# Kernel optimization log

Hardware: AMD Instinct MI355X
Metric: run time of the kernel (lower is better)

The kernel has to match this reference:

```python
import jax, jax.numpy as jnp
import numpy as np

B, T, E, H = 2, 2048, 1024, 16
DV = E // H
EPS = 1e-5

def _layernorm(x, g, b):
    m = jnp.mean(x, axis=-1, keepdims=True)
    v = jnp.mean((x - m) ** 2, axis=-1, keepdims=True)
    return (x - m) * jax.lax.rsqrt(v + EPS) * g + b

def setup_inputs() -> dict:
    key = jax.random.key(0)
    ks = jax.random.split(key, 10)
    s = lambda fan_in: 1.0 / np.sqrt(fan_in)
    return {
        "x": jax.random.normal(ks[0], (B, T, E), jnp.float32),
        "wq": jax.random.normal(ks[1], (H, E, DV), jnp.float32) * s(E),
        "wk": jax.random.normal(ks[2], (H, E, DV), jnp.float32) * s(E),
        "wv": jax.random.normal(ks[3], (H, E, DV), jnp.float32) * s(E),
        "w_proj": jax.random.normal(ks[4], (E, E), jnp.float32) * s(E),
        "b_proj": jnp.zeros((E,), jnp.float32),
        "w1": jax.random.normal(ks[5], (E, 4 * E), jnp.float32) * s(E),
        "b1": jnp.zeros((4 * E,), jnp.float32),
        "w2": jax.random.normal(ks[6], (4 * E, E), jnp.float32) * s(4 * E),
        "b2": jnp.zeros((E,), jnp.float32),
        "g1": jnp.ones((E,), jnp.float32),
        "be1": jnp.zeros((E,), jnp.float32),
        "g2": jnp.ones((E,), jnp.float32),
        "be2": jnp.zeros((E,), jnp.float32),
    }

def reference(x, wq, wk, wv, w_proj, b_proj, w1, b1, w2, b2, g1, be1, g2, be2):
    Bc, Tc, C = x.shape
    # --- masked multi-head self-attention on pre-LN input ---
    h = _layernorm(x, g1, be1)
    q = jnp.einsum('bte,hed->bhtd', h, wq)
    k = jnp.einsum('bte,hed->bhtd', h, wk)
    v = jnp.einsum('bte,hed->bhtd', h, wv)
    # NOTE: original scales by C**-0.5 where C = full embed dim (not head dim)
    scores = jnp.einsum('bhtd,bhsd->bhts', q, k) * (C ** -0.5)
    causal = jnp.tril(jnp.ones((Tc, Tc), bool))
    scores = jnp.where(causal, scores, jnp.float32(-jnp.inf))
    probs = jax.nn.softmax(scores, axis=-1)  # dropout is identity in eval
    attn = jnp.einsum('bhts,bhsd->bhtd', probs, v)
    attn = attn.transpose(0, 2, 1, 3).reshape(Bc, Tc, C)
    x = x + (attn @ w_proj + b_proj)
    # --- feed-forward ---
    h2 = _layernorm(x, g2, be2)
    ff = jax.nn.relu(h2 @ w1 + b1) @ w2 + b2
    return x + ff
```

## Files before the change

### kernel.cpp

```cpp
#include <hip/hip_runtime.h>
#include <hip/hip_bf16.h>

typedef __bf16 bf16x8 __attribute__((ext_vector_type(8)));
typedef __bf16 bf16x4 __attribute__((ext_vector_type(4)));
typedef float f32x4 __attribute__((ext_vector_type(4)));

#define T_SEQ 2048
#define EMB 1024
#define NH 16
#define DV 64

__device__ __forceinline__ void gload16(const __bf16* g, __bf16* l) {
    __builtin_amdgcn_global_load_lds(
        (const __attribute__((address_space(1))) unsigned int*)g,
        (__attribute__((address_space(3))) unsigned int*)l, 16, 0, 0);
}

__global__ void transpose_cvt(const float* __restrict__ src, __bf16* __restrict__ dst,
                              int R, int C, long src_bstride, long dst_bstride, float scale) {
    __shared__ float tile[32][33];
    const int b = blockIdx.z;
    const float* s = src + (long)b * src_bstride;
    __bf16* d = dst + (long)b * dst_bstride;
    const int c0 = blockIdx.x * 32, r0 = blockIdx.y * 32;
    #pragma unroll
    for (int i = threadIdx.y; i < 32; i += 8)
        tile[i][threadIdx.x] = s[(long)(r0 + i) * C + c0 + threadIdx.x];
    __syncthreads();
    #pragma unroll
    for (int i = threadIdx.y; i < 32; i += 8)
        d[(long)(c0 + i) * R + r0 + threadIdx.x] = (__bf16)(tile[threadIdx.x][i] * scale);
}

__global__ void vt_transpose(const __bf16* __restrict__ qkv, __bf16* __restrict__ Vt) {
    __shared__ __bf16 tile[64][72];
    const int bh = blockIdx.y, b = bh >> 4, h = bh & 15;
    const int t0 = blockIdx.x * 64;
    const __bf16* src = qkv + (long)b * T_SEQ * 3072 + 2048 + h * 64;
    const int tt = threadIdx.x >> 3, seg = threadIdx.x & 7;
    #pragma unroll
    for (int half = 0; half < 2; half++) {
        const int t = half * 32 + tt;
        bf16x8 v = *reinterpret_cast<const bf16x8*>(src + (long)(t0 + t) * 3072 + seg * 8);
        *reinterpret_cast<bf16x8*>(&tile[t][seg * 8]) = v;
    }
    __syncthreads();
    __bf16* dst = Vt + (long)bh * 64 * T_SEQ + t0;
    #pragma unroll
    for (int half = 0; half < 2; half++) {
        const int d = half * 32 + tt;
        bf16x8 v;
        #pragma unroll
        for (int i = 0; i < 8; i++) v[i] = tile[seg * 8 + i][d];
        *reinterpret_cast<bf16x8*>(dst + (long)d * T_SEQ + seg * 8) = v;
    }
}

__global__ void ln_kernel(const float* __restrict__ x, const float* __restrict__ g,
                          const float* __restrict__ be, __bf16* __restrict__ out) {
    const int row = blockIdx.x;
    const float4 xv = reinterpret_cast<const float4*>(x + (long)row * EMB)[threadIdx.x];
    float s = xv.x + xv.y + xv.z + xv.w;
    float sq = xv.x * xv.x + xv.y * xv.y + xv.z * xv.z + xv.w * xv.w;
    #pragma unroll
    for (int off = 32; off; off >>= 1) { s += __shfl_down(s, off); sq += __shfl_down(sq, off); }
    __shared__ float red[8];
    const int w = threadIdx.x >> 6, lane = threadIdx.x & 63;
    if (lane == 0) { red[w] = s; red[4 + w] = sq; }
    __syncthreads();
    if (threadIdx.x == 0) {
        float st = red[0] + red[1] + red[2] + red[3];
        float sqt = red[4] + red[5] + red[6] + red[7];
        float mean = st * (1.0f / EMB);
        float var = sqt * (1.0f / EMB) - mean * mean;
        red[0] = mean; red[1] = rsqrtf(var + 1e-5f);
    }
    __syncthreads();
    const float mean = red[0], rstd = red[1];
    const float4 gv = reinterpret_cast<const float4*>(g)[threadIdx.x];
    const float4 bv = reinterpret_cast<const float4*>(be)[threadIdx.x];
    bf16x4 o;
    o[0] = (__bf16)((xv.x - mean) * rstd * gv.x + bv.x);
    o[1] = (__bf16)((xv.y - mean) * rstd * gv.y + bv.y);
    o[2] = (__bf16)((xv.z - mean) * rstd * gv.z + bv.z);
    o[3] = (__bf16)((xv.w - mean) * rstd * gv.w + bv.w);
    *reinterpret_cast<bf16x4*>(out + (long)row * EMB + threadIdx.x * 4) = o;
}

template <int BN, int OUT_BF16, int RELU, int HAS_BIAS, int HAS_RES>
__global__ __launch_bounds__(256)
void gemm_nt(const __bf16* __restrict__ A, const __bf16* __restrict__ BT,
             const float* __restrict__ bias, const float* __restrict__ res,
             void* __restrict__ outp, int M, int N, int K) {
    constexpr int NFN = BN / 32;
    __shared__ __align__(16) __bf16 As[128 * 64];
    __shared__ __align__(16) __bf16 Bs[BN * 64];
    const int t = threadIdx.x;
    const int w = t >> 6, lane = t & 63;
    const int wm = (w >> 1) * 64, wn = (w & 1) * (BN / 2);
    const int m0 = blockIdx.y * 128, n0 = blockIdx.x * BN;
    const int rA = lane & 15, kA = (lane >> 4) * 8;
    const int srow = t >> 3;
    const int scol = (t & 7) * 8;

    const __bf16* Ab = A + (long)(m0 + srow) * K + scol;
    const __bf16* Bb = BT + (long)(n0 + srow) * K + scol;
    __bf16* Asw = As + srow * 64 + scol;
    __bf16* Bsw = Bs + srow * 64 + scol;

    f32x4 acc[4][NFN] = {};
    for (int k0 = 0; k0 < K; k0 += 64) {
        #pragma unroll
        for (int i = 0; i < 4; i++)
            gload16(Ab + (long)(32 * i) * K + k0, Asw + 32 * i * 64);
        #pragma unroll
        for (int i = 0; i < BN / 32; i++)
            gload16(Bb + (long)(32 * i) * K + k0, Bsw + 32 * i * 64);
        __syncthreads();
        #pragma unroll
        for (int kk = 0; kk < 2; kk++) {
            bf16x8 af[4], bfr[NFN];
            #pragma unroll
            for (int m = 0; m < 4; m++)
                af[m] = *reinterpret_cast<const bf16x8*>(As + (wm + m * 16 + rA) * 64 + kk * 32 + kA);
            #pragma unroll
            for (int n = 0; n < NFN; n++)
                bfr[n] = *reinterpret_cast<const bf16x8*>(Bs + (wn + n * 16 + rA) * 64 + kk * 32 + kA);
            #pragma unroll
            for (int m = 0; m < 4; m++)
                #pragma unroll
                for (int n = 0; n < NFN; n++)
                    acc[m][n] = __builtin_amdgcn_mfma_f32_16x16x32_bf16(af[m], bfr[n], acc[m][n], 0, 0, 0);
        }
        __syncthreads();
    }
    const int rl = (lane >> 4) * 4, cl = lane & 15;
    #pragma unroll
    for (int m = 0; m < 4; m++) {
        #pragma unroll
        for (int n = 0; n < NFN; n++) {
            const int gc = n0 + wn + n * 16 + cl;
            float bval = 0.0f;
            if (HAS_BIAS) bval = bias[gc];
            #pragma unroll
            for (int r = 0; r < 4; r++) {
                const int gr = m0 + wm + m * 16 + rl + r;
                float v = acc[m][n][r] + bval;
                if (HAS_RES) v += res[(long)gr * N + gc];
                if (RELU) v = fmaxf(v, 0.0f);
                if (OUT_BF16) ((__bf16*)outp)[(long)gr * N + gc] = (__bf16)v;
                else          ((float*)outp)[(long)gr * N + gc] = v;
            }
        }
    }
}

template <int MASKED>
__device__ __forceinline__ void attn_compute(
    const char* __restrict__ Kl, const char* __restrict__ Vl,
    __bf16 (*__restrict__ PsW)[72],
    const bf16x8 (&qf)[2][2], const bf16x8& ones,
    f32x4 (&o)[2][4], f32x4 (&l5)[2], float (&mr)[2][4],
    int kv0, int rA, int g, int rl, int qw)
{
    const int swz = (rA & 7) << 4;
    bf16x8 kf[4][2];
    #pragma unroll
    for (int c = 0; c < 4; c++)
        #pragma unroll
        for (int kc = 0; kc < 2; kc++)
            kf[c][kc] = *reinterpret_cast<const bf16x8*>(
                Kl + (c * 16 + rA) * 128 + ((kc * 64 + g * 16) ^ swz));
    f32x4 sa[2][4];
    #pragma unroll
    for (int rt = 0; rt < 2; rt++)
        #pragma unroll
        for (int c = 0; c < 4; c++) {
            f32x4 acc = {};
            acc = __builtin_amdgcn_mfma_f32_16x16x32_bf16(qf[rt][0], kf[c][0], acc, 0, 0, 0);
            acc = __builtin_amdgcn_mfma_f32_16x16x32_bf16(qf[rt][1], kf[c][1], acc, 0, 0, 0);
            sa[rt][c] = acc;
        }
    #pragma unroll
    for (int rt = 0; rt < 2; rt++) {
        #pragma unroll
        for (int r = 0; r < 4; r++) {
            float s0 = sa[rt][0][r], s1 = sa[rt][1][r], s2 = sa[rt][2][r], s3 = sa[rt][3][r];
            if (MASKED) {
                const int gr = qw + rt * 16 + rl + r;
                if (kv0 + rA > gr)      s0 = -__builtin_inff();
                if (kv0 + 16 + rA > gr) s1 = -__builtin_inff();
                if (kv0 + 32 + rA > gr) s2 = -__builtin_inff();
                if (kv0 + 48 + rA > gr) s3 = -__builtin_inff();
            }
            float tm = fmaxf(fmaxf(s0, s1), fmaxf(s2, s3));
            #pragma unroll
            for (int msk = 1; msk < 16; msk <<= 1) tm = fmaxf(tm, __shfl_xor(tm, msk));
            const float mo = mr[rt][r];
            const float mn = fmaxf(mo, tm);
            mr[rt][r] = mn;
            const float sc = __expf(mo - mn);
            const float p0 = __expf(s0 - mn);
            const float p1 = __expf(s1 - mn);
            const float p2 = __expf(s2 - mn);
            const float p3 = __expf(s3 - mn);
            #pragma unroll
            for (int n = 0; n < 4; n++) o[rt][n][r] *= sc;
            l5[rt][r] *= sc;
            const int prow = rt * 16 + rl + r;
            PsW[prow][rA]      = (__bf16)p0;
            PsW[prow][16 + rA] = (__bf16)p1;
            PsW[prow][32 + rA] = (__bf16)p2;
            PsW[prow][48 + rA] = (__bf16)p3;
        }
    }
    asm volatile("s_waitcnt lgkmcnt(0)" ::: "memory");

    bf16x8 ap[2][2];
    #pragma unroll
    for (int rt = 0; rt < 2; rt++)
        #pragma unroll
        for (int ks = 0; ks < 2; ks++)
            ap[rt][ks] = *reinterpret_cast<const bf16x8*>(&PsW[rt * 16 + rA][ks * 32 + g * 8]);
    #pragma unroll
    for (int ks = 0; ks < 2; ks++) {
        #pragma unroll
        for (int rt = 0; rt < 2; rt++)
            l5[rt] = __builtin_amdgcn_mfma_f32_16x16x32_bf16(ap[rt][ks], ones, l5[rt], 0, 0, 0);
        #pragma unroll
        for (int n = 0; n < 4; n++) {
            bf16x8 bv = *reinterpret_cast<const bf16x8*>(
                Vl + (n * 16 + rA) * 128 + ((ks * 64 + g * 16) ^ swz));
            #pragma unroll
            for (int rt = 0; rt < 2; rt++)
                o[rt][n] = __builtin_amdgcn_mfma_f32_16x16x32_bf16(ap[rt][ks], bv, o[rt][n], 0, 0, 0);
        }
    }
}

__global__ __launch_bounds__(256)
void attn_kernel(const __bf16* __restrict__ qkv, const __bf16* __restrict__ Vt,
                 __bf16* __restrict__ attn) {
    __shared__ __bf16 Ks[2][64 * 64];
    __shared__ __bf16 Vs[2][64 * 64];
    __shared__ __bf16 Ps[4][32][72];

    const int bh = blockIdx.y, b = bh >> 4, h = bh & 15;
    const int qtile = (int)gridDim.x - 1 - (int)blockIdx.x;
    const int q0 = qtile * 128;
    const int w = threadIdx.x >> 6, lane = threadIdx.x & 63;
    const int qw = q0 + w * 32;
    const int rA = lane & 15, g = lane >> 4, rl = g * 4;
    const int srow8 = lane >> 3;
    const int scol = (lane & 7) * 16;
    const int wcol = scol ^ (srow8 << 4);

    const char* qb = (const char*)(qkv + (long)b * T_SEQ * 3072 + h * 64);
    const char* kb = qb + 2048;
    const char* vtb = (const char*)(Vt + (long)bh * 64 * T_SEQ);

    bf16x8 qf[2][2];
    #pragma unroll
    for (int rt = 0; rt < 2; rt++)
        #pragma unroll
        for (int kc = 0; kc < 2; kc++)
            qf[rt][kc] = *reinterpret_cast<const bf16x8*>(
                qb + (long)(qw + rt * 16 + rA) * 6144 + kc * 64 + g * 16);

    bf16x8 ones;
    #pragma unroll
    for (int i = 0; i < 8; i++) ones[i] = (__bf16)1.0f;

    f32x4 o[2][4] = {};
    f32x4 l5[2] = {};
    float mr[2][4];
    #pragma unroll
    for (int rt = 0; rt < 2; rt++)
        #pragma unroll
        for (int r = 0; r < 4; r++) mr[rt][r] = -__builtin_inff();

    const int nsteps = q0 / 64 + 2;
    const int t_avail = qw + 32;
    const int isK = (w < 2);
    const int r0 = (w & 1) * 32 + srow8;

    bf16x8 stg[4];
    auto issue = [&](int kv0) {
        if (isK) {
            #pragma unroll
            for (int i = 0; i < 4; i++)
                stg[i] = *reinterpret_cast<const bf16x8*>(kb + (long)(kv0 + r0 + i * 8) * 6144 + scol);
        } else {
            #pragma unroll
            for (int i = 0; i < 4; i++)
                stg[i] = *reinterpret_cast<const bf16x8*>(vtb + (long)(r0 + i * 8) * 4096 + kv0 * 2 + scol);
        }
    };
    auto lwrite = [&](int buf) {
        char* base = isK ? (char*)Ks[buf] : (char*)Vs[buf];
        #pragma unroll
        for (int i = 0; i < 4; i++)
            *reinterpret_cast<bf16x8*>(base + (r0 + i * 8) * 128 + wcol) = stg[i];
    };

    issue(0);
    lwrite(0);
    __syncthreads();

    for (int t = 0; t < nsteps; ++t) {
        const int kv0 = t * 64, cur = t & 1;
        const bool has_next = (t + 1 < nsteps);
        if (has_next) issue(kv0 + 64);
        if (kv0 < t_avail) {
            if (kv0 + 64 <= qw)
                attn_compute<0>((const char*)Ks[cur], (const char*)Vs[cur], Ps[w],
                                qf, ones, o, l5, mr, kv0, rA, g, rl, qw);
            else
                attn_compute<1>((const char*)Ks[cur], (const char*)Vs[cur], Ps[w],
                                qf, ones, o, l5, mr, kv0, rA, g, rl, qw);
        }
        if (has_next) lwrite(cur ^ 1);
        __syncthreads();
    }

    #pragma unroll
    for (int rt = 0; rt < 2; rt++)
        #pragma unroll
        for (int n = 0; n < 4; n++)
            #pragma unroll
            for (int r = 0; r < 4; r++) {
                const int gr = qw + rt * 16 + rl + r;
                attn[(long)(b * T_SEQ + gr) * EMB + h * 64 + n * 16 + rA] =
                    (__bf16)(o[rt][n][r] / l5[rt][r]);
            }
}

extern "C" void kernel_launch(void* const* d_in, const int* in_sizes, int n_in,
                              void* d_out, int out_size, void* d_ws, size_t ws_size,
                              hipStream_t stream) {
    const float* x      = (const float*)d_in[0];
    const float* wq     = (const float*)d_in[1];
    const float* wk     = (const float*)d_in[2];
    const float* wv     = (const float*)d_in[3];
    const float* w_proj = (const float*)d_in[4];
    const float* b_proj = (const float*)d_in[5];
    const float* w1     = (const float*)d_in[6];
    const float* b1     = (const float*)d_in[7];
    const float* w2     = (const float*)d_in[8];
    const float* b2     = (const float*)d_in[9];
    const float* g1     = (const float*)d_in[10];
    const float* be1    = (const float*)d_in[11];
    const float* g2     = (const float*)d_in[12];
    const float* be2    = (const float*)d_in[13];
    float* out = (float*)d_out;

    char* ws = (char*)d_ws;
    __bf16* WqkvT = (__bf16*)ws;  ws += 3072L * 1024 * 2;
    __bf16* WprojT = (__bf16*)ws; ws += 1024L * 1024 * 2;
    __bf16* W1T = (__bf16*)ws;    ws += 4096L * 1024 * 2;
    __bf16* W2T = (__bf16*)ws;    ws += 1024L * 4096 * 2;
    __bf16* h1  = (__bf16*)ws;    ws += 4096L * 1024 * 2;
    __bf16* qkvb = (__bf16*)ws;
    __bf16* attnb = (__bf16*)(ws + 4096L * 3072 * 2);
    __bf16* ffb = (__bf16*)ws;    ws += 4096L * 3072 * 2 + 4096L * 1024 * 2;
    float* x2 = (float*)ws;
    __bf16* Vt = (__bf16*)ws;

    const dim3 tb(32, 8);
    transpose_cvt<<<dim3(2, 32, 16), tb, 0, stream>>>(wq, WqkvT,                1024, 64, 65536L, 65536L, 0.03125f);
    transpose_cvt<<<dim3(2, 32, 16), tb, 0, stream>>>(wk, WqkvT + 1024L * 1024, 1024, 64, 65536L, 65536L, 1.0f);
    transpose_cvt<<<dim3(2, 32, 16), tb, 0, stream>>>(wv, WqkvT + 2048L * 1024, 1024, 64, 65536L, 65536L, 1.0f);
    transpose_cvt<<<dim3(32, 32, 1),  tb, 0, stream>>>(w_proj, WprojT, 1024, 1024, 0, 0, 1.0f);
    transpose_cvt<<<dim3(128, 32, 1), tb, 0, stream>>>(w1, W1T, 1024, 4096, 0, 0, 1.0f);
    transpose_cvt<<<dim3(32, 128, 1), tb, 0, stream>>>(w2, W2T, 4096, 1024, 0, 0, 1.0f);

    ln_kernel<<<4096, 256, 0, stream>>>(x, g1, be1, h1);
    gemm_nt<128, 1, 0, 0, 0><<<dim3(24, 32), 256, 0, stream>>>(h1, WqkvT, nullptr, nullptr, qkvb, 4096, 3072, 1024);
    vt_transpose<<<dim3(32, 32), 256, 0, stream>>>(qkvb, Vt);
    attn_kernel<<<dim3(16, 32), 256, 0, stream>>>(qkvb, Vt, attnb);
    gemm_nt<64, 0, 0, 1, 1><<<dim3(16, 32), 256, 0, stream>>>(attnb, WprojT, b_proj, x, x2, 4096, 1024, 1024);
    ln_kernel<<<4096, 256, 0, stream>>>(x2, g2, be2, h1);
    gemm_nt<128, 1, 1, 1, 0><<<dim3(32, 32), 256, 0, stream>>>(h1, W1T, b1, nullptr, ffb, 4096, 4096, 1024);
    gemm_nt<64, 0, 0, 1, 1><<<dim3(16, 32), 256, 0, stream>>>(ffb, W2T, b2, x2, out, 4096, 1024, 4096);
}
```

Before: 443.5 us.

## Swizzle GEMM LDS tiles, add MFMA priority hints, remap attention blocks across XCDs

The GEMM kernel now loads each 16-byte chunk with an XOR swizzle by row, and the fragment reads apply the matching XOR. This is meant to remove LDS bank conflicts on the bf16x8 reads. The attention kernel wraps its QK and PV MFMA sections in s_setprio(1)/s_setprio(0) so those waves get issue priority. It also launches as a 1D grid and remaps block IDs so consecutive heads and q-tiles spread across the 8 XCDs while heavy causal tiles still go first. The remap changes cache locality per XCD and assumes the hardware dispatches blocks round-robin across XCDs.

```diff
diff --git a/kernel.cpp b/kernel.cpp
--- a/kernel.cpp
+++ b/kernel.cpp
@@ -100,13 +100,15 @@
     const int wm = (w >> 1) * 64, wn = (w & 1) * (BN / 2);
     const int m0 = blockIdx.y * 128, n0 = blockIdx.x * BN;
     const int rA = lane & 15, kA = (lane >> 4) * 8;
+    const int swzr = (rA & 7) * 8;
     const int srow = t >> 3;
-    const int scol = (t & 7) * 8;
-
-    const __bf16* Ab = A + (long)(m0 + srow) * K + scol;
-    const __bf16* Bb = BT + (long)(n0 + srow) * K + scol;
-    __bf16* Asw = As + srow * 64 + scol;
-    __bf16* Bsw = Bs + srow * 64 + scol;
+    const int chunk = t & 7;
+    const int schunk = chunk ^ (srow & 7);
+
+    const __bf16* Ab = A + (long)(m0 + srow) * K + schunk * 8;
+    const __bf16* Bb = BT + (long)(n0 + srow) * K + schunk * 8;
+    __bf16* Asw = As + srow * 64 + chunk * 8;
+    __bf16* Bsw = Bs + srow * 64 + chunk * 8;
 
     f32x4 acc[4][NFN] = {};
     for (int k0 = 0; k0 < K; k0 += 64) {
@@ -122,10 +124,12 @@
             bf16x8 af[4], bfr[NFN];
             #pragma unroll
             for (int m = 0; m < 4; m++)
-                af[m] = *reinterpret_cast<const bf16x8*>(As + (wm + m * 16 + rA) * 64 + kk * 32 + kA);
+                af[m] = *reinterpret_cast<const bf16x8*>(
+                    As + (wm + m * 16 + rA) * 64 + ((kk * 32 + kA) ^ swzr));
             #pragma unroll
             for (int n = 0; n < NFN; n++)
-                bfr[n] = *reinterpret_cast<const bf16x8*>(Bs + (wn + n * 16 + rA) * 64 + kk * 32 + kA);
+                bfr[n] = *reinterpret_cast<const bf16x8*>(
+                    Bs + (wn + n * 16 + rA) * 64 + ((kk * 32 + kA) ^ swzr));
             #pragma unroll
             for (int m = 0; m < 4; m++)
                 #pragma unroll
@@ -172,6 +176,7 @@
             kf[c][kc] = *reinterpret_cast<const bf16x8*>(
                 Kl + (c * 16 + rA) * 128 + ((kc * 64 + g * 16) ^ swz));
     f32x4 sa[2][4];
+    __builtin_amdgcn_s_setprio(1);
     #pragma unroll
     for (int rt = 0; rt < 2; rt++)
         #pragma unroll
@@ -181,6 +186,7 @@
             acc = __builtin_amdgcn_mfma_f32_16x16x32_bf16(qf[rt][1], kf[c][1], acc, 0, 0, 0);
             sa[rt][c] = acc;
         }
+    __builtin_amdgcn_s_setprio(0);
     #pragma unroll
     for (int rt = 0; rt < 2; rt++) {
         #pragma unroll
@@ -222,6 +228,7 @@
         #pragma unroll
         for (int ks = 0; ks < 2; ks++)
             ap[rt][ks] = *reinterpret_cast<const bf16x8*>(&PsW[rt * 16 + rA][ks * 32 + g * 8]);
+    __builtin_amdgcn_s_setprio(1);
     #pragma unroll
     for (int ks = 0; ks < 2; ks++) {
         #pragma unroll
@@ -236,6 +243,7 @@
                 o[rt][n] = __builtin_amdgcn_mfma_f32_16x16x32_bf16(ap[rt][ks], bv, o[rt][n], 0, 0, 0);
         }
     }
+    __builtin_amdgcn_s_setprio(0);
 }
 
 __global__ __launch_bounds__(256)
@@ -245,8 +253,10 @@
     __shared__ __bf16 Vs[2][64 * 64];
     __shared__ __bf16 Ps[4][32][72];
 
-    const int bh = blockIdx.y, b = bh >> 4, h = bh & 15;
-    const int qtile = (int)gridDim.x - 1 - (int)blockIdx.x;
+    const int bid = (int)blockIdx.x;
+    const int wgid = (bid & 7) * 64 + (bid >> 3);
+    const int bh = wgid >> 4, b = bh >> 4, h = bh & 15;
+    const int qtile = 15 - (wgid & 15);
     const int q0 = qtile * 128;
     const int w = threadIdx.x >> 6, lane = threadIdx.x & 63;
     const int qw = q0 + w * 32;
@@ -377,7 +387,7 @@
     ln_kernel<<<4096, 256, 0, stream>>>(x, g1, be1, h1);
     gemm_nt<128, 1, 0, 0, 0><<<dim3(24, 32), 256, 0, stream>>>(h1, WqkvT, nullptr, nullptr, qkvb, 4096, 3072, 1024);
     vt_transpose<<<dim3(32, 32), 256, 0, stream>>>(qkvb, Vt);
-    attn_kernel<<<dim3(16, 32), 256, 0, stream>>>(qkvb, Vt, attnb);
+    attn_kernel<<<512, 256, 0, stream>>>(qkvb, Vt, attnb);
     gemm_nt<64, 0, 0, 1, 1><<<dim3(16, 32), 256, 0, stream>>>(attnb, WprojT, b_proj, x, x2, 4096, 1024, 1024);
     ln_kernel<<<4096, 256, 0, stream>>>(x2, g2, be2, h1);
     gemm_nt<128, 1, 1, 1, 0><<<dim3(32, 32), 256, 0, stream>>>(h1, W1T, b1, nullptr, ffb, 4096, 4096, 1024);
```

New measurement: 407.7 us. -8.1%, faster.
